# Kernel tuning notes

Measured on AMD Instinct MI355X. Metric: run time of the kernel, lower is better.

The kernel has to match this reference:

```python
import jax, jax.numpy as jnp
import numpy as np

B, T, H = 64, 32, 768          # batch, num query tokens, hidden
E, NB, DFF = 8, 2, 3072        # num_experts, num_beams, expert ffn dim


def setup_inputs() -> dict:
    key = jax.random.key(0)
    ks = jax.random.split(key, 6)
    x = jax.random.normal(ks[0], (B, T, H), dtype=jnp.float32)
    gate_w = jax.random.normal(ks[1], (E, H), dtype=jnp.float32) * 0.02
    w1 = jax.random.normal(ks[2], (E, DFF, H), dtype=jnp.float32) * 0.02
    b1 = jnp.zeros((E, DFF), dtype=jnp.float32)
    w2 = jax.random.normal(ks[3], (E, H, DFF), dtype=jnp.float32) * 0.02
    b2 = jnp.zeros((E, H), dtype=jnp.float32)
    return {"x": x, "gate_w": gate_w, "w1": w1, "b1": b1, "w2": w2, "b2": b2}


def reference(x, gate_w, w1, b1, w2, b2):
    # ---- forward_gate: attention_mask is all ones -> plain mean over tokens ----
    x_avg = jnp.mean(x, axis=1)                         # [B, H]
    logits_gate = x_avg @ gate_w.T                      # [B, E]
    current_scores = jax.nn.softmax(logits_gate, axis=-1)

    # ---- importance auxiliary loss (torch.std is unbiased, ddof=1) ----
    importance = jnp.sum(current_scores, axis=0)        # [E]
    importance_loss = (jnp.std(importance, ddof=1) / jnp.mean(importance)) ** 2

    # ---- beam_search, first layer: exp(log(scores)) == scores; topk num_beams ----
    topk_vals, topk_idx = jax.lax.top_k(current_scores, NB)   # [B, NB]
    beam_scores = topk_vals.reshape(B * NB)
    expert_route = topk_idx.reshape(B * NB, 1).astype(jnp.int32)
    beam_idx = jnp.arange(B * NB, dtype=jnp.int32)

    # ---- replicate x / scores per beam: unsqueeze+expand+view == repeat ----
    x_rep = jnp.repeat(x, NB, axis=0)                   # [B*NB, T, H]
    scores_rep = jnp.repeat(current_scores, NB, axis=0) # [B*NB, E]
    input_x = x_rep[beam_idx]                           # identity gather (faithful)

    # ---- forward_expert_ffn: run ALL experts, then one-hot * prob combine ----
    h = jnp.einsum('bth,efh->betf', input_x, w1) + b1[None, :, None, :]
    h = jax.nn.gelu(h, approximate=False)               # torch nn.GELU default (exact)
    cand = jnp.einsum('betf,ehf->beth', h, w2) + b2[None, :, None, :]  # [B*NB, E, T, H]

    sel = expert_route[:, -1]                           # [B*NB]
    onehot = jax.nn.one_hot(sel, E, dtype=cand.dtype)   # [B*NB, E]
    weights = scores_rep * onehot                       # weight_type == 'ffn_prob'
    output = jnp.einsum('beth,be->bth', cand, weights)  # [B*NB, T, H]

    return output, beam_scores, expert_route, beam_idx, importance_loss
```

## Files before the change

### kernel.cpp

```cpp
#include <hip/hip_runtime.h>
#include <hip/hip_bf16.h>
#include <math.h>

#define Bsz 64
#define T 32
#define H 768
#define E 8
#define NB 2
#define DFF 3072
#define NBEAM (Bsz * NB)
#define NT8MAX 24

#define OUT_BS 3145728
#define OUT_ER 3145856
#define OUT_BI 3145984
#define OUT_IL 3146112

#define WS_LOGITS 0
#define WS_BEAMW  1536
#define WS_SORT   1664
#define WS_T8E    1792
#define WS_T8B    1832
#define WS_T8C    1872
#define WS_XBF    2048
#define WS_HBF    (2048 + 786432)

typedef __attribute__((ext_vector_type(8))) short short8;
typedef __attribute__((ext_vector_type(4))) float f32x4;

__device__ __forceinline__ short8 cvt8(const float4 u, const float4 v) {
    union { short8 s; unsigned w[4]; } r;
    __hip_bfloat162 t;
    t = __float22bfloat162_rn(make_float2(u.x, u.y)); r.w[0] = *(unsigned*)&t;
    t = __float22bfloat162_rn(make_float2(u.z, u.w)); r.w[1] = *(unsigned*)&t;
    t = __float22bfloat162_rn(make_float2(v.x, v.y)); r.w[2] = *(unsigned*)&t;
    t = __float22bfloat162_rn(make_float2(v.z, v.w)); r.w[3] = *(unsigned*)&t;
    return r.s;
}

__device__ __forceinline__ void async16(void* lds, const void* g) {
    __builtin_amdgcn_global_load_lds(
        (const __attribute__((address_space(1))) void*)g,
        (__attribute__((address_space(3))) void*)lds, 16, 0, 0);
}

__global__ __launch_bounds__(256) void conv_x_kernel(
    const float* __restrict__ x, ushort* __restrict__ xb, int n4)
{
    const int i = blockIdx.x * 256 + threadIdx.x;
    if (i >= n4) return;
    const float4 v = ((const float4*)x)[i];
    __hip_bfloat162 t0 = __float22bfloat162_rn(make_float2(v.x, v.y));
    __hip_bfloat162 t1 = __float22bfloat162_rn(make_float2(v.z, v.w));
    ushort4 o;
    o.x = (*(unsigned*)&t0) & 0xffff; o.y = (*(unsigned*)&t0) >> 16;
    o.z = (*(unsigned*)&t1) & 0xffff; o.w = (*(unsigned*)&t1) >> 16;
    ((ushort4*)xb)[i] = o;
}

__global__ __launch_bounds__(256) void gate_partial_kernel(
    const float* __restrict__ x, const float* __restrict__ gate_w,
    float* __restrict__ logits_part)
{
    __shared__ float part[4][E];
    const int chunk = blockIdx.x, b = blockIdx.y;
    const int tid = threadIdx.x, wv = tid >> 6, lane = tid & 63;
    const int c = chunk * 256 + tid;
    const float* xp = x + (size_t)b * T * H + c;
    float s = 0.f;
    #pragma unroll
    for (int t = 0; t < T; ++t) s += xp[t * H];
    const float avg = s * (1.0f / T);
    #pragma unroll
    for (int e = 0; e < E; ++e) {
        float p = avg * gate_w[e * H + c];
        #pragma unroll
        for (int off = 32; off; off >>= 1) p += __shfl_down(p, off, 64);
        if (lane == 0) part[wv][e] = p;
    }
    __syncthreads();
    if (tid < E) {
        float t = part[0][tid] + part[1][tid] + part[2][tid] + part[3][tid];
        logits_part[chunk * 512 + b * E + tid] = t;
    }
}

__global__ __launch_bounds__(64) void gating_kernel(
    const float* __restrict__ logits_part, float* __restrict__ beam_w,
    int* __restrict__ sortb, int* __restrict__ t8e, int* __restrict__ t8b,
    int* __restrict__ t8c, float* __restrict__ dout)
{
    const int r = threadIdx.x;
    float v[E];
    float mx = -1e30f;
    #pragma unroll
    for (int e = 0; e < E; ++e) {
        v[e] = logits_part[r * E + e] + logits_part[512 + r * E + e]
             + logits_part[1024 + r * E + e];
        mx = fmaxf(mx, v[e]);
    }
    float s = 0.f;
    #pragma unroll
    for (int e = 0; e < E; ++e) { v[e] = expf(v[e] - mx); s += v[e]; }
    const float inv = 1.0f / s;
    #pragma unroll
    for (int e = 0; e < E; ++e) v[e] *= inv;
    float v0 = -1.f, v1 = -1.f; int i0 = 0, i1 = 0;
    #pragma unroll
    for (int e = 0; e < E; ++e) {
        if (v[e] > v0)      { v1 = v0; i1 = i0; v0 = v[e]; i0 = e; }
        else if (v[e] > v1) { v1 = v[e]; i1 = e; }
    }
    const int b0 = 2 * r, b1 = 2 * r + 1;
    dout[OUT_BS + b0] = v0;          dout[OUT_BS + b1] = v1;
    dout[OUT_ER + b0] = (float)i0;   dout[OUT_ER + b1] = (float)i1;
    dout[OUT_BI + b0] = (float)b0;   dout[OUT_BI + b1] = (float)b1;
    beam_w[b0] = v0;  beam_w[b1] = v1;
    float imp[E];
    #pragma unroll
    for (int e = 0; e < E; ++e) {
        float t = v[e];
        #pragma unroll
        for (int off = 1; off < 64; off <<= 1) t += __shfl_xor(t, off, 64);
        imp[e] = t;
    }
    if (r == 0) {
        float tot = 0.f;
        #pragma unroll
        for (int e = 0; e < E; ++e) tot += imp[e];
        const float mean = tot / E;
        float var = 0.f;
        #pragma unroll
        for (int e = 0; e < E; ++e) { float d = imp[e] - mean; var += d * d; }
        var /= (E - 1);
        dout[OUT_IL] = var / (mean * mean);
    }
    unsigned long long m0[E], m1[E];
    #pragma unroll
    for (int e = 0; e < E; ++e) {
        m0[e] = __ballot(i0 == e);
        m1[e] = __ballot(i1 == e);
    }
    int cnt[E], off[E];
    int a0 = 0;
    #pragma unroll
    for (int e = 0; e < E; ++e) {
        cnt[e] = __popcll(m0[e]) + __popcll(m1[e]);
        off[e] = a0; a0 += cnt[e];
    }
    const unsigned long long below = (r == 0) ? 0ull : ((1ull << r) - 1ull);
    const unsigned long long incl  = below | (1ull << r);
    const int pos0 = __popcll(m0[i0] & below) + __popcll(m1[i0] & below);
    const int pos1 = __popcll(m0[i1] & incl)  + __popcll(m1[i1] & below);
    sortb[off[i0] + pos0] = b0;
    sortb[off[i1] + pos1] = b1;
    if (r == 0) {
        int tiles[E];
        int used[NT8MAX];
        for (int t = 0; t < NT8MAX; ++t) used[t] = 0;
        #pragma unroll
        for (int e = 0; e < E; ++e) tiles[e] = (cnt[e] + 7) >> 3;
        #pragma unroll
        for (int e = 0; e < E; ++e) {
            const int k = tiles[e] < 3 ? tiles[e] : 3;
            for (int i = 0; i < k; ++i) {
                const int sl = 3 * e + i;
                t8e[sl] = e; t8b[sl] = off[e] + 8 * i;
                const int rem = cnt[e] - 8 * i;
                t8c[sl] = rem < 8 ? rem : 8;
                used[sl] = 1;
            }
        }
        int fs[NT8MAX]; int nf = 0;
        for (int round = 0; round < 3; ++round)
            for (int c = 0; c < E; ++c) {
                const int sl = 3 * c + round;
                if (!used[sl]) fs[nf++] = sl;
            }
        int fp = 0;
        for (int e = 0; e < E; ++e)
            for (int i = 3; i < tiles[e]; ++i) {
                const int sl = fs[fp++];
                t8e[sl] = e; t8b[sl] = off[e] + 8 * i;
                const int rem = cnt[e] - 8 * i;
                t8c[sl] = rem < 8 ? rem : 8;
                used[sl] = 1;
            }
        for (int t = 0; t < NT8MAX; ++t) if (!used[t]) t8c[t] = 0;
    }
}

template <int KTOT, bool DO_GELU>
__global__ __launch_bounds__(256, 2) void moe_ffn_mfma(
    const ushort* __restrict__ Abf, int a_div,
    const float* __restrict__ Wf32, int w_rows,
    const float* __restrict__ biasb,
    const int* __restrict__ sortb, const int* __restrict__ t8e,
    const int* __restrict__ t8b, const int* __restrict__ t8c,
    const float* __restrict__ beam_w,
    void* __restrict__ Obase)
{
    constexpr int KT = KTOT / 32;
    __shared__ __align__(16) ushort sA[2][256 * 32];
    __shared__ __align__(16) ushort sB[2][64 * 32];

    const int nx  = gridDim.x;
    const int hw  = blockIdx.y * nx + blockIdx.x;
    const int xcd = hw & 7;
    const int j   = hw >> 3;
    const int tile  = 3 * xcd + j % 3;
    const int strip = j / 3;

    const int cnt  = t8c[tile];
    if (cnt == 0) return;
    const int e    = t8e[tile];
    const int base = t8b[tile];
    const int tid  = threadIdx.x;
    const int wv   = tid >> 6;
    const int lane = tid & 63;
    const int quad = lane >> 4;
    const int l16  = lane & 15;
    const int mh   = (wv & 1) * 128;
    const int nh   = (wv >> 1) * 32;
    const int n0   = strip * 64;

    int bm[8];
    #pragma unroll
    for (int s = 0; s < 8; ++s) bm[s] = sortb[base + (s < cnt ? s : cnt - 1)];

    const ushort* aseg[4];
    #pragma unroll
    for (int jj = 0; jj < 4; ++jj) {
        const int s = (wv * 4 + jj) * 64 + lane;
        const int r = s >> 2;
        const int c = (s & 3) ^ ((s >> 3) & 3);
        aseg[jj] = Abf + (size_t)(bm[r >> 5] / a_div) * T * KTOT
                 + (size_t)(r & 31) * KTOT + c * 8;
    }
    const float* wseg;
    int wslot;
    {
        const int r = tid >> 2;
        const int c = (tid & 3) ^ ((tid >> 3) & 3);
        wseg  = Wf32 + (size_t)e * w_rows * KTOT + (size_t)(n0 + r) * KTOT + c * 8;
        wslot = tid * 8;
    }

    const int fx = (l16 >> 1) & 3;
    int aoff[8], boff[2];
    #pragma unroll
    for (int mt = 0; mt < 8; ++mt)
        aoff[mt] = (mh + mt * 16 + l16) * 32 + ((quad ^ fx) * 8);
    #pragma unroll
    for (int nt = 0; nt < 2; ++nt)
        boff[nt] = (nh + nt * 16 + l16) * 32 + ((quad ^ fx) * 8);

    float4 wr0 = *(const float4*)(wseg);
    float4 wr1 = *(const float4*)(wseg + 4);
    #pragma unroll
    for (int jj = 0; jj < 4; ++jj)
        async16((char*)sA[0] + (wv * 4 + jj) * 1024, aseg[jj]);

    f32x4 acc[8][2];
    #pragma unroll
    for (int mt = 0; mt < 8; ++mt) {
        acc[mt][0] = {0.f, 0.f, 0.f, 0.f};
        acc[mt][1] = {0.f, 0.f, 0.f, 0.f};
    }

    for (int kt = 0; kt < KT; ++kt) {
        const int p = kt & 1;
        *(short8*)(sB[p] + wslot) = cvt8(wr0, wr1);
        __syncthreads();
        if (kt + 1 < KT) {
            const int kn = (kt + 1) * 32;
            #pragma unroll
            for (int jj = 0; jj < 4; ++jj)
                async16((char*)sA[1 - p] + (wv * 4 + jj) * 1024, aseg[jj] + kn);
            wr0 = *(const float4*)(wseg + kn);
            wr1 = *(const float4*)(wseg + kn + 4);
        }
        const short8 wf0 = *(const short8*)(sB[p] + boff[0]);
        const short8 wf1 = *(const short8*)(sB[p] + boff[1]);
        #pragma unroll
        for (int mt = 0; mt < 8; ++mt) {
            const short8 af = *(const short8*)(sA[p] + aoff[mt]);
            acc[mt][0] = __builtin_amdgcn_mfma_f32_16x16x32_bf16(
                af, wf0, acc[mt][0], 0, 0, 0);
            acc[mt][1] = __builtin_amdgcn_mfma_f32_16x16x32_bf16(
                af, wf1, acc[mt][1], 0, 0, 0);
        }
    }

    #pragma unroll
    for (int nt = 0; nt < 2; ++nt) {
        const int n = n0 + nh + nt * 16 + l16;
        const float bias = biasb[(size_t)e * w_rows + n];
        #pragma unroll
        for (int mt = 0; mt < 8; ++mt) {
            const int rowb = mh + mt * 16 + quad * 4;
            const int s = rowb >> 5;
            if (s >= cnt) continue;
            const int b = bm[s];
            const float scale = DO_GELU ? 1.0f : beam_w[b];
            #pragma unroll
            for (int r = 0; r < 4; ++r) {
                const int t = (rowb + r) & 31;
                float vv = acc[mt][nt][r] + bias;
                const size_t idx = (size_t)b * T * w_rows + (size_t)t * w_rows + n;
                if (DO_GELU) {
                    vv = 0.5f * vv * (1.0f + erff(vv * 0.70710678118654752f));
                    ((__hip_bfloat16*)Obase)[idx] = __float2bfloat16(vv);
                } else {
                    ((float*)Obase)[idx] = vv * scale;
                }
            }
        }
    }
}

extern "C" void kernel_launch(void* const* d_in, const int* in_sizes, int n_in,
                              void* d_out, int out_size, void* d_ws, size_t ws_size,
                              hipStream_t stream)
{
    const float* x      = (const float*)d_in[0];
    const float* gate_w = (const float*)d_in[1];
    const float* w1     = (const float*)d_in[2];
    const float* b1     = (const float*)d_in[3];
    const float* w2     = (const float*)d_in[4];
    const float* b2     = (const float*)d_in[5];
    float* out = (float*)d_out;
    float* ws  = (float*)d_ws;

    float*  logits = ws + WS_LOGITS;
    float*  beam_w = ws + WS_BEAMW;
    int*    sortb  = (int*)(ws + WS_SORT);
    int*    t8e    = (int*)(ws + WS_T8E);
    int*    t8b    = (int*)(ws + WS_T8B);
    int*    t8c    = (int*)(ws + WS_T8C);
    ushort* x_bf   = (ushort*)(ws + WS_XBF);
    ushort* h_bf   = (ushort*)(ws + WS_HBF);

    conv_x_kernel<<<(Bsz * T * H / 4 + 255) / 256, 256, 0, stream>>>(
        x, x_bf, Bsz * T * H / 4);
    gate_partial_kernel<<<dim3(3, Bsz), 256, 0, stream>>>(x, gate_w, logits);
    gating_kernel<<<1, 64, 0, stream>>>(logits, beam_w, sortb, t8e, t8b, t8c, out);
    moe_ffn_mfma<H, true><<<dim3(DFF / 64, NT8MAX), 256, 0, stream>>>(
        x_bf, NB, w1, DFF, b1, sortb, t8e, t8b, t8c, beam_w, (void*)h_bf);
    moe_ffn_mfma<DFF, false><<<dim3(H / 64, NT8MAX), 256, 0, stream>>>(
        h_bf, 1, w2, H, b2, sortb, t8e, t8b, t8c, beam_w, out);
}
```

Measured before the change: 375.2 us.

## Widen MoE GEMM N-tile, split-K the second GEMM, fuse x conversion into gating

The x-to-bf16 conversion now happens inside the gating partial-sum kernel, which removes one launch and a second pass over x. The MoE FFN kernel takes a 128-wide N tile, so each A tile is reused across more output columns. The second GEMM is split four ways along K, with atomicAdd accumulation into a pre-zeroed output, to give that smaller grid more parallelism. In exchange it adds a memset, float atomics that make the sum order nondeterministic, and more accumulator registers per wave.

```diff
diff --git a/kernel.cpp b/kernel.cpp
--- a/kernel.cpp
+++ b/kernel.cpp
@@ -44,32 +44,27 @@
         (__attribute__((address_space(3))) void*)lds, 16, 0, 0);
 }
 
-__global__ __launch_bounds__(256) void conv_x_kernel(
-    const float* __restrict__ x, ushort* __restrict__ xb, int n4)
-{
-    const int i = blockIdx.x * 256 + threadIdx.x;
-    if (i >= n4) return;
-    const float4 v = ((const float4*)x)[i];
-    __hip_bfloat162 t0 = __float22bfloat162_rn(make_float2(v.x, v.y));
-    __hip_bfloat162 t1 = __float22bfloat162_rn(make_float2(v.z, v.w));
-    ushort4 o;
-    o.x = (*(unsigned*)&t0) & 0xffff; o.y = (*(unsigned*)&t0) >> 16;
-    o.z = (*(unsigned*)&t1) & 0xffff; o.w = (*(unsigned*)&t1) >> 16;
-    ((ushort4*)xb)[i] = o;
-}
-
-__global__ __launch_bounds__(256) void gate_partial_kernel(
+__global__ __launch_bounds__(256) void gate_conv_kernel(
     const float* __restrict__ x, const float* __restrict__ gate_w,
-    float* __restrict__ logits_part)
+    ushort* __restrict__ xb, float* __restrict__ logits_part)
 {
     __shared__ float part[4][E];
     const int chunk = blockIdx.x, b = blockIdx.y;
     const int tid = threadIdx.x, wv = tid >> 6, lane = tid & 63;
     const int c = chunk * 256 + tid;
     const float* xp = x + (size_t)b * T * H + c;
+    ushort* xo = xb + (size_t)b * T * H + c;
     float s = 0.f;
     #pragma unroll
-    for (int t = 0; t < T; ++t) s += xp[t * H];
+    for (int t = 0; t < T; t += 2) {
+        const float f0 = xp[t * H];
+        const float f1 = xp[(t + 1) * H];
+        s += f0; s += f1;
+        __hip_bfloat162 t2 = __float22bfloat162_rn(make_float2(f0, f1));
+        const unsigned u = *(const unsigned*)&t2;
+        xo[t * H]       = (ushort)(u & 0xffff);
+        xo[(t + 1) * H] = (ushort)(u >> 16);
+    }
     const float avg = s * (1.0f / T);
     #pragma unroll
     for (int e = 0; e < E; ++e) {
@@ -190,7 +185,7 @@
     }
 }
 
-template <int KTOT, bool DO_GELU>
+template <int KTOT, int NTILE, bool DO_GELU, int NSLICE>
 __global__ __launch_bounds__(256, 2) void moe_ffn_mfma(
     const ushort* __restrict__ Abf, int a_div,
     const float* __restrict__ Wf32, int w_rows,
@@ -200,16 +195,22 @@
     const float* __restrict__ beam_w,
     void* __restrict__ Obase)
 {
-    constexpr int KT = KTOT / 32;
+    constexpr int KSPAN = KTOT / NSLICE;
+    constexpr int KT    = KSPAN / 32;
+    constexpr int NFRAG = NTILE / 32;
+    constexpr int WSLOT = NTILE / 64;
     __shared__ __align__(16) ushort sA[2][256 * 32];
-    __shared__ __align__(16) ushort sB[2][64 * 32];
+    __shared__ __align__(16) ushort sB[2][NTILE * 32];
 
     const int nx  = gridDim.x;
+    const int nwg = nx * gridDim.y;
     const int hw  = blockIdx.y * nx + blockIdx.x;
-    const int xcd = hw & 7;
-    const int j   = hw >> 3;
-    const int tile  = 3 * xcd + j % 3;
-    const int strip = j / 3;
+    const int q8  = nwg >> 3;
+    const int lid = (hw & 7) * q8 + (hw >> 3);
+    const int tile  = lid % NT8MAX;
+    const int rr    = lid / NT8MAX;
+    const int strip = rr % nx;
+    const int k0    = (rr / nx) * KSPAN;
 
     const int cnt  = t8c[tile];
     if (cnt == 0) return;
@@ -221,8 +222,8 @@
     const int quad = lane >> 4;
     const int l16  = lane & 15;
     const int mh   = (wv & 1) * 128;
-    const int nh   = (wv >> 1) * 32;
-    const int n0   = strip * 64;
+    const int nh   = (wv >> 1) * (NTILE / 2);
+    const int n0   = strip * NTILE;
 
     int bm[8];
     #pragma unroll
@@ -235,65 +236,78 @@
         const int r = s >> 2;
         const int c = (s & 3) ^ ((s >> 3) & 3);
         aseg[jj] = Abf + (size_t)(bm[r >> 5] / a_div) * T * KTOT
-                 + (size_t)(r & 31) * KTOT + c * 8;
-    }
-    const float* wseg;
-    int wslot;
-    {
-        const int r = tid >> 2;
-        const int c = (tid & 3) ^ ((tid >> 3) & 3);
-        wseg  = Wf32 + (size_t)e * w_rows * KTOT + (size_t)(n0 + r) * KTOT + c * 8;
-        wslot = tid * 8;
+                 + (size_t)(r & 31) * KTOT + c * 8 + k0;
+    }
+    const float* wseg[WSLOT];
+    int wslot[WSLOT];
+    #pragma unroll
+    for (int jj = 0; jj < WSLOT; ++jj) {
+        const int s = jj * 256 + tid;
+        const int r = s >> 2;
+        const int c = (s & 3) ^ ((s >> 3) & 3);
+        wseg[jj] = Wf32 + (size_t)e * w_rows * KTOT + (size_t)(n0 + r) * KTOT
+                 + c * 8 + k0;
+        wslot[jj] = s * 8;
     }
 
     const int fx = (l16 >> 1) & 3;
-    int aoff[8], boff[2];
+    int aoff[8], boff[NFRAG];
     #pragma unroll
     for (int mt = 0; mt < 8; ++mt)
         aoff[mt] = (mh + mt * 16 + l16) * 32 + ((quad ^ fx) * 8);
     #pragma unroll
-    for (int nt = 0; nt < 2; ++nt)
+    for (int nt = 0; nt < NFRAG; ++nt)
         boff[nt] = (nh + nt * 16 + l16) * 32 + ((quad ^ fx) * 8);
 
-    float4 wr0 = *(const float4*)(wseg);
-    float4 wr1 = *(const float4*)(wseg + 4);
+    float4 wr[WSLOT][2];
+    #pragma unroll
+    for (int jj = 0; jj < WSLOT; ++jj) {
+        wr[jj][0] = *(const float4*)(wseg[jj]);
+        wr[jj][1] = *(const float4*)(wseg[jj] + 4);
+    }
     #pragma unroll
     for (int jj = 0; jj < 4; ++jj)
         async16((char*)sA[0] + (wv * 4 + jj) * 1024, aseg[jj]);
 
-    f32x4 acc[8][2];
-    #pragma unroll
-    for (int mt = 0; mt < 8; ++mt) {
-        acc[mt][0] = {0.f, 0.f, 0.f, 0.f};
-        acc[mt][1] = {0.f, 0.f, 0.f, 0.f};
-    }
+    f32x4 acc[8][NFRAG];
+    #pragma unroll
+    for (int mt = 0; mt < 8; ++mt)
+        #pragma unroll
+        for (int nt = 0; nt < NFRAG; ++nt) acc[mt][nt] = {0.f, 0.f, 0.f, 0.f};
 
     for (int kt = 0; kt < KT; ++kt) {
         const int p = kt & 1;
-        *(short8*)(sB[p] + wslot) = cvt8(wr0, wr1);
+        #pragma unroll
+        for (int jj = 0; jj < WSLOT; ++jj)
+            *(short8*)(sB[p] + wslot[jj]) = cvt8(wr[jj][0], wr[jj][1]);
         __syncthreads();
         if (kt + 1 < KT) {
             const int kn = (kt + 1) * 32;
             #pragma unroll
             for (int jj = 0; jj < 4; ++jj)
                 async16((char*)sA[1 - p] + (wv * 4 + jj) * 1024, aseg[jj] + kn);
-            wr0 = *(const float4*)(wseg + kn);
-            wr1 = *(const float4*)(wseg + kn + 4);
+            #pragma unroll
+            for (int jj = 0; jj < WSLOT; ++jj) {
+                wr[jj][0] = *(const float4*)(wseg[jj] + kn);
+                wr[jj][1] = *(const float4*)(wseg[jj] + kn + 4);
+            }
         }
-        const short8 wf0 = *(const short8*)(sB[p] + boff[0]);
-        const short8 wf1 = *(const short8*)(sB[p] + boff[1]);
+        short8 wf[NFRAG];
+        #pragma unroll
+        for (int nt = 0; nt < NFRAG; ++nt)
+            wf[nt] = *(const short8*)(sB[p] + boff[nt]);
         #pragma unroll
         for (int mt = 0; mt < 8; ++mt) {
             const short8 af = *(const short8*)(sA[p] + aoff[mt]);
-            acc[mt][0] = __builtin_amdgcn_mfma_f32_16x16x32_bf16(
-                af, wf0, acc[mt][0], 0, 0, 0);
-            acc[mt][1] = __builtin_amdgcn_mfma_f32_16x16x32_bf16(
-                af, wf1, acc[mt][1], 0, 0, 0);
+            #pragma unroll
+            for (int nt = 0; nt < NFRAG; ++nt)
+                acc[mt][nt] = __builtin_amdgcn_mfma_f32_16x16x32_bf16(
+                    af, wf[nt], acc[mt][nt], 0, 0, 0);
         }
     }
 
     #pragma unroll
-    for (int nt = 0; nt < 2; ++nt) {
+    for (int nt = 0; nt < NFRAG; ++nt) {
         const int n = n0 + nh + nt * 16 + l16;
         const float bias = biasb[(size_t)e * w_rows + n];
         #pragma unroll
@@ -306,13 +320,14 @@
             #pragma unroll
             for (int r = 0; r < 4; ++r) {
                 const int t = (rowb + r) & 31;
-                float vv = acc[mt][nt][r] + bias;
                 const size_t idx = (size_t)b * T * w_rows + (size_t)t * w_rows + n;
                 if (DO_GELU) {
+                    float vv = acc[mt][nt][r] + bias;
                     vv = 0.5f * vv * (1.0f + erff(vv * 0.70710678118654752f));
                     ((__hip_bfloat16*)Obase)[idx] = __float2bfloat16(vv);
                 } else {
-                    ((float*)Obase)[idx] = vv * scale;
+                    float vv = acc[mt][nt][r] + ((k0 == 0) ? bias : 0.f);
+                    atomicAdd((float*)Obase + idx, vv * scale);
                 }
             }
         }
@@ -341,12 +356,12 @@
     ushort* x_bf   = (ushort*)(ws + WS_XBF);
     ushort* h_bf   = (ushort*)(ws + WS_HBF);
 
-    conv_x_kernel<<<(Bsz * T * H / 4 + 255) / 256, 256, 0, stream>>>(
-        x, x_bf, Bsz * T * H / 4);
-    gate_partial_kernel<<<dim3(3, Bsz), 256, 0, stream>>>(x, gate_w, logits);
+    hipMemsetAsync(out, 0, (size_t)NBEAM * T * H * sizeof(float), stream);
+
+    gate_conv_kernel<<<dim3(3, Bsz), 256, 0, stream>>>(x, gate_w, x_bf, logits);
     gating_kernel<<<1, 64, 0, stream>>>(logits, beam_w, sortb, t8e, t8b, t8c, out);
-    moe_ffn_mfma<H, true><<<dim3(DFF / 64, NT8MAX), 256, 0, stream>>>(
+    moe_ffn_mfma<H, 128, true, 1><<<dim3(DFF / 128, NT8MAX), 256, 0, stream>>>(
         x_bf, NB, w1, DFF, b1, sortb, t8e, t8b, t8c, beam_w, (void*)h_bf);
-    moe_ffn_mfma<DFF, false><<<dim3(H / 64, NT8MAX), 256, 0, stream>>>(
+    moe_ffn_mfma<DFF, 128, false, 4><<<dim3(H / 128, NT8MAX * 4), 256, 0, stream>>>(
         h_bf, 1, w2, H, b2, sortb, t8e, t8b, t8c, beam_w, out);
 }
```

After: 316.4 us. -15.7%, faster.
